# Performance work log

Measured on AMD Instinct MI355X. Metric: run time of the kernel, lower is better.

## Reference

```python
import jax, jax.numpy as jnp
import numpy as np

N = 4096      # nodes
IN = 45       # input_dim
H = 44        # hidden_dim
NH = 4        # num_heads
HD = H // NH  # head_dim = 11
E = 131072    # edges
SCALE = 0.1
NEG = -1e9


def _linear_params(key, fan_in, fan_out):
    kw, kb = jax.random.split(key)
    s = 1.0 / np.sqrt(fan_in)
    W = jax.random.uniform(kw, (fan_in, fan_out), jnp.float32, -s, s)
    b = jax.random.uniform(kb, (fan_out,), jnp.float32, -s, s)
    return W, b


def setup_inputs() -> dict:
    key = jax.random.key(0)
    ks = jax.random.split(key, 9)
    node_features = jax.random.normal(ks[0], (N, IN), jnp.float32)
    edge_index = jax.random.randint(ks[1], (2, E), 0, N, jnp.int32)
    # dt_minutes must be nonnegative (sqrt); channel 1 unused by forward
    temporal_data = jax.random.uniform(ks[2], (N, N, 2), jnp.float32, 0.01, 60.0)
    Wp, bp = _linear_params(ks[3], IN, H)
    Wq, bq = _linear_params(ks[4], H, H)
    Wk, bk = _linear_params(ks[5], H, H)
    Wv, bv = _linear_params(ks[6], H, H)
    Wo, bo = _linear_params(ks[7], H, H)
    return dict(node_features=node_features, edge_index=edge_index,
                temporal_data=temporal_data, Wp=Wp, bp=bp, Wq=Wq, bq=bq,
                Wk=Wk, bk=bk, Wv=Wv, bv=bv, Wo=Wo, bo=bo)


def reference(node_features, edge_index, temporal_data,
              Wp, bp, Wq, bq, Wk, bk, Wv, bv, Wo, bo):
    # input projection (N > 1000 so dag_positional_encoding is skipped)
    x = node_features @ Wp + bp                       # [N, H]
    # per-head QKV: [NH, N, HD]
    Q = (x @ Wq + bq).reshape(N, NH, HD).transpose(1, 0, 2)
    K = (x @ Wk + bk).reshape(N, NH, HD).transpose(1, 0, 2)
    V = (x @ Wv + bv).reshape(N, NH, HD).transpose(1, 0, 2)
    # edge mask: True blocks attention; edges and self-loops are allowed
    mask = jnp.ones((N, N), dtype=bool)
    mask = mask.at[edge_index[0], edge_index[1]].set(False)
    diag = jnp.arange(N)
    mask = mask.at[diag, diag].set(False)
    # rbf temporal bias: -sqrt(dt / (scale + 1e-6))
    tb = -jnp.sqrt(temporal_data[:, :, 0] / (SCALE + 1e-6))  # [N, N]
    scores = jnp.einsum('hnd,hmd->hnm', Q, K) / np.sqrt(HD)  # [NH, N, N]
    scores = scores + tb[None]
    scores = jnp.where(mask[None], NEG, scores)
    attn = jax.nn.softmax(scores, axis=-1)
    out = jnp.einsum('hnm,hmd->hnd', attn, V)                # [NH, N, HD]
    attended = out.transpose(1, 0, 2).reshape(N, H)          # [N, H]
    return attended @ Wo + bo
```

## Files before the change

kernel.cpp:

```cpp
#include <hip/hip_runtime.h>
#include <math.h>

#define NN 4096
#define INDIM 45
#define HH 44
#define NHEAD 4
#define HD 11
#define NEDGE 131072
#define CAP 128
#define MASKW (NN / 64)
#define NPB 8
#define RPITCH 66
#define KVSTRIDE 24

typedef unsigned short ushort_t;

__device__ __forceinline__ float wsum64(float v) {
    #pragma unroll
    for (int i = 32; i > 0; i >>= 1) v += __shfl_xor(v, i, 64);
    return v;
}
__device__ __forceinline__ float wmax64(float v) {
    #pragma unroll
    for (int i = 32; i > 0; i >>= 1) v = fmaxf(v, __shfl_xor(v, i, 64));
    return v;
}
__device__ __forceinline__ ushort_t f2bf(float x) {
    unsigned u = __float_as_uint(x);
    u += 0x7FFFu + ((u >> 16) & 1u);
    return (ushort_t)(u >> 16);
}
__device__ __forceinline__ float bfl(unsigned u) { return __uint_as_float(u << 16); }
__device__ __forceinline__ float bfh(unsigned u) { return __uint_as_float(u & 0xFFFF0000u); }

__global__ __launch_bounds__(256)
void proj_zero(const float* __restrict__ nf,
               const float* __restrict__ Wp, const float* __restrict__ bp,
               const float* __restrict__ Wq, const float* __restrict__ bq,
               const float* __restrict__ Wk, const float* __restrict__ bk,
               const float* __restrict__ Wv, const float* __restrict__ bv,
               unsigned long long* __restrict__ mask,
               float* __restrict__ Qp, ushort_t* __restrict__ KVb) {
    const int tid = threadIdx.x;
    const int gsz = gridDim.x * 256;
    for (int i = blockIdx.x * 256 + tid; i < NN * MASKW; i += gsz) mask[i] = 0ull;

    __shared__ float xs[NPB][HH];
    const int n0 = blockIdx.x * NPB;
    for (int idx = tid; idx < NPB * HH; idx += 256) {
        int nl = idx / HH, j = idx - nl * HH;
        const float* row = nf + (size_t)(n0 + nl) * INDIM;
        float a = bp[j];
        #pragma unroll
        for (int k = 0; k < INDIM; ++k) a += row[k] * Wp[k * HH + j];
        xs[nl][j] = a;
    }
    __syncthreads();
    for (int idx = tid; idx < NPB * HH; idx += 256) {
        int nl = idx / HH, j = idx - nl * HH;
        const float* row = xs[nl];
        float aq = bq[j], ak = bk[j], av = bv[j];
        #pragma unroll
        for (int k = 0; k < HH; ++k) {
            float xv = row[k];
            aq += xv * Wq[k * HH + j];
            ak += xv * Wk[k * HH + j];
            av += xv * Wv[k * HH + j];
        }
        int h = j / HD, d = j - h * HD;
        size_t nh = (size_t)(n0 + nl) * NHEAD + h;
        Qp[nh * 12 + d]             = aq;
        KVb[nh * KVSTRIDE + d]      = f2bf(ak);
        KVb[nh * KVSTRIDE + 12 + d] = f2bf(av);
    }
}

__global__ __launch_bounds__(256)
void build_mask(const int* __restrict__ ei, unsigned long long* __restrict__ mask) {
    int i = blockIdx.x * blockDim.x + threadIdx.x;
    if (i < NEDGE) {
        int r = ei[i];
        int c = ei[NEDGE + i];
        atomicOr(&mask[(size_t)r * MASKW + (c >> 6)], 1ull << (c & 63));
    }
}

__global__ __launch_bounds__(256, 6)
void attn_out(const float* __restrict__ Qp, const ushort_t* __restrict__ KVb,
              const float* __restrict__ temporal,
              const unsigned long long* __restrict__ mask,
              const float* __restrict__ Wo, const float* __restrict__ bo,
              float* __restrict__ out) {
    const int tid = threadIdx.x;
    const int lane = tid & 63;
    const int h = tid >> 6;
    const int n = blockIdx.x;
    const float scale = 0.30151134457776363f;
    const float tbmul = 9.99990000099999f;

    __shared__ int cols_s[NHEAD][CAP];
    __shared__ float red_s[NHEAD][12][RPITCH];
    __shared__ float att_s[HH];

    unsigned long long w = mask[(size_t)n * MASKW + lane];
    if (lane == (n >> 6)) w |= 1ull << (n & 63);
    int c = __popcll(w);
    int inc = c;
    #pragma unroll
    for (int i = 1; i < 64; i <<= 1) {
        int v = __shfl_up(inc, i, 64);
        if (lane >= i) inc += v;
    }
    int off = inc - c;
    int deg = __shfl(inc, 63, 64);
    if (deg > CAP) deg = CAP;
    while (w) {
        int b = __builtin_ctzll(w);
        w &= w - 1;
        if (off < CAP) cols_s[h][off] = lane * 64 + b;
        ++off;
    }

    const float4* qp4 = (const float4*)(Qp + ((size_t)n * NHEAD + h) * 12);
    float4 q0 = qp4[0], q1 = qp4[1], q2 = qp4[2];

    if (deg <= 64) {
        const bool act = lane < deg;
        const int col = act ? cols_s[h][lane] : cols_s[h][0];
        float t = temporal[((size_t)n * NN + col) * 2];
        const uint4* kv4 = (const uint4*)(KVb + (size_t)(col * NHEAD + h) * KVSTRIDE);
        uint4 A = kv4[0], B = kv4[1], C = kv4[2];
        float s = q0.x*bfl(A.x) + q0.y*bfh(A.x) + q0.z*bfl(A.y) + q0.w*bfh(A.y)
                + q1.x*bfl(A.z) + q1.y*bfh(A.z) + q1.z*bfl(A.w) + q1.w*bfh(A.w)
                + q2.x*bfl(B.x) + q2.y*bfh(B.x) + q2.z*bfl(B.y);
        float p = act ? __expf(s * scale - sqrtf(t * tbmul)) : 0.f;
        float vv[11] = { bfl(B.z), bfh(B.z), bfl(B.w), bfh(B.w),
                         bfl(C.x), bfh(C.x), bfl(C.y), bfh(C.y),
                         bfl(C.z), bfh(C.z), bfl(C.w) };

        float* myred = &red_s[h][0][0];
        #pragma unroll
        for (int d = 0; d < HD; ++d) myred[d * RPITCH + lane] = p * vv[d];
        myred[11 * RPITCH + lane] = p;
        int dd = lane < 12 ? lane : 0;
        const float2* rp = (const float2*)(myred + dd * RPITCH);
        float sum = 0.f;
        #pragma unroll
        for (int i = 0; i < 32; ++i) { float2 v2 = rp[i]; sum += v2.x + v2.y; }
        float inv = 1.f / __shfl(sum, 11, 64);
        if (lane < HD) att_s[h * HD + lane] = sum * inv;
    } else {
        float mcur = -INFINITY, lsum = 0.f, oacc[HD];
        #pragma unroll
        for (int d = 0; d < HD; ++d) oacc[d] = 0.f;
        for (int base = 0; base < deg; base += 64) {
            const int jj = base + lane;
            const bool act = jj < deg;
            const int col = act ? cols_s[h][jj] : 0;
            float t = temporal[((size_t)n * NN + col) * 2];
            const uint4* kv4 = (const uint4*)(KVb + (size_t)(col * NHEAD + h) * KVSTRIDE);
            uint4 A = kv4[0], B = kv4[1], C = kv4[2];
            float s = q0.x*bfl(A.x) + q0.y*bfh(A.x) + q0.z*bfl(A.y) + q0.w*bfh(A.y)
                    + q1.x*bfl(A.z) + q1.y*bfh(A.z) + q1.z*bfl(A.w) + q1.w*bfh(A.w)
                    + q2.x*bfl(B.x) + q2.y*bfh(B.x) + q2.z*bfl(B.y);
            float vv[11] = { bfl(B.z), bfh(B.z), bfl(B.w), bfh(B.w),
                             bfl(C.x), bfh(C.x), bfl(C.y), bfh(C.y),
                             bfl(C.z), bfh(C.z), bfl(C.w) };
            if (act) {
                s = s * scale - sqrtf(t * tbmul);
                if (s > mcur) {
                    float f = __expf(mcur - s);
                    lsum *= f;
                    #pragma unroll
                    for (int d = 0; d < HD; ++d) oacc[d] *= f;
                    mcur = s;
                }
                float p = __expf(s - mcur);
                lsum += p;
                #pragma unroll
                for (int d = 0; d < HD; ++d) oacc[d] += p * vv[d];
            }
        }
        float M = wmax64(mcur);
        float sc = (mcur == -INFINITY) ? 0.f : __expf(mcur - M);
        float L = wsum64(lsum * sc);
        float inv = 1.f / L;
        #pragma unroll
        for (int d = 0; d < HD; ++d) {
            float o = wsum64(oacc[d] * sc);
            if (lane == d) att_s[h * HD + d] = o * inv;
        }
    }
    __syncthreads();

    if (tid < HH) {
        float a = bo[tid];
        #pragma unroll
        for (int k = 0; k < HH; ++k) a += att_s[k] * Wo[k * HH + tid];
        out[(size_t)n * HH + tid] = a;
    }
}

extern "C" void kernel_launch(void* const* d_in, const int* in_sizes, int n_in,
                              void* d_out, int out_size, void* d_ws, size_t ws_size,
                              hipStream_t stream) {
    const float* nf       = (const float*)d_in[0];
    const int*   ei       = (const int*)d_in[1];
    const float* temporal = (const float*)d_in[2];
    const float* Wp = (const float*)d_in[3];
    const float* bp = (const float*)d_in[4];
    const float* Wq = (const float*)d_in[5];
    const float* bq = (const float*)d_in[6];
    const float* Wk = (const float*)d_in[7];
    const float* bk = (const float*)d_in[8];
    const float* Wv = (const float*)d_in[9];
    const float* bv = (const float*)d_in[10];
    const float* Wo = (const float*)d_in[11];
    const float* bo = (const float*)d_in[12];
    float* outp = (float*)d_out;

    char* ws = (char*)d_ws;
    unsigned long long* mask = (unsigned long long*)ws;
    float*    Qp  = (float*)(ws + (2u << 20));
    ushort_t* KVb = (ushort_t*)(Qp + (size_t)NN * NHEAD * 12);

    proj_zero<<<NN / NPB, 256, 0, stream>>>(nf, Wp, bp, Wq, bq, Wk, bk, Wv, bv,
                                            mask, Qp, KVb);
    build_mask<<<(NEDGE + 255) / 256, 256, 0, stream>>>(ei, mask);
    attn_out<<<NN, 256, 0, stream>>>(Qp, KVb, temporal, mask, Wo, bo, outp);
}
```

Measured before the change: 33.65 us.

## Split attention into per-head 64-thread blocks and separate output projection kernel

The attention kernel now launches one 64-thread block per (node, head) instead of one 256-thread block per node, which removes the block-wide barrier and lets heads schedule independently. Attended values go to a workspace buffer, and a new kernel applies the Wo projection. In exchange there is an extra kernel launch and a global round-trip for the attended tensor. The mask word popcount and scan are now repeated per head-block, though they already ran once per wavefront before.

```diff
diff --git a/kernel.cpp b/kernel.cpp
--- a/kernel.cpp
+++ b/kernel.cpp
@@ -85,22 +85,22 @@
     }
 }
 
-__global__ __launch_bounds__(256, 6)
-void attn_out(const float* __restrict__ Qp, const ushort_t* __restrict__ KVb,
-              const float* __restrict__ temporal,
-              const unsigned long long* __restrict__ mask,
-              const float* __restrict__ Wo, const float* __restrict__ bo,
-              float* __restrict__ out) {
-    const int tid = threadIdx.x;
-    const int lane = tid & 63;
-    const int h = tid >> 6;
-    const int n = blockIdx.x;
+__global__ __launch_bounds__(64, 6)
+void attn64(const float* __restrict__ Qp, const ushort_t* __restrict__ KVb,
+            const float* __restrict__ temporal,
+            const unsigned long long* __restrict__ mask,
+            float* __restrict__ att) {
+    const int lane = threadIdx.x;
+    const int n = blockIdx.x >> 2;
+    const int h = blockIdx.x & 3;
     const float scale = 0.30151134457776363f;
     const float tbmul = 9.99990000099999f;
 
-    __shared__ int cols_s[NHEAD][CAP];
-    __shared__ float red_s[NHEAD][12][RPITCH];
-    __shared__ float att_s[HH];
+    __shared__ int cols_s[CAP];
+    __shared__ float red_s[12][RPITCH];
+
+    const float4* qp4 = (const float4*)(Qp + ((size_t)n * NHEAD + h) * 12);
+    float4 q0 = qp4[0], q1 = qp4[1], q2 = qp4[2];
 
     unsigned long long w = mask[(size_t)n * MASKW + lane];
     if (lane == (n >> 6)) w |= 1ull << (n & 63);
@@ -117,16 +117,13 @@
     while (w) {
         int b = __builtin_ctzll(w);
         w &= w - 1;
-        if (off < CAP) cols_s[h][off] = lane * 64 + b;
+        if (off < CAP) cols_s[off] = lane * 64 + b;
         ++off;
     }
-
-    const float4* qp4 = (const float4*)(Qp + ((size_t)n * NHEAD + h) * 12);
-    float4 q0 = qp4[0], q1 = qp4[1], q2 = qp4[2];
 
     if (deg <= 64) {
         const bool act = lane < deg;
-        const int col = act ? cols_s[h][lane] : cols_s[h][0];
+        const int col = act ? cols_s[lane] : cols_s[0];
         float t = temporal[((size_t)n * NN + col) * 2];
         const uint4* kv4 = (const uint4*)(KVb + (size_t)(col * NHEAD + h) * KVSTRIDE);
         uint4 A = kv4[0], B = kv4[1], C = kv4[2];
@@ -138,17 +135,16 @@
                          bfl(C.x), bfh(C.x), bfl(C.y), bfh(C.y),
                          bfl(C.z), bfh(C.z), bfl(C.w) };
 
-        float* myred = &red_s[h][0][0];
-        #pragma unroll
-        for (int d = 0; d < HD; ++d) myred[d * RPITCH + lane] = p * vv[d];
-        myred[11 * RPITCH + lane] = p;
+        #pragma unroll
+        for (int d = 0; d < HD; ++d) red_s[d][lane] = p * vv[d];
+        red_s[11][lane] = p;
         int dd = lane < 12 ? lane : 0;
-        const float2* rp = (const float2*)(myred + dd * RPITCH);
+        const float2* rp = (const float2*)(&red_s[dd][0]);
         float sum = 0.f;
         #pragma unroll
         for (int i = 0; i < 32; ++i) { float2 v2 = rp[i]; sum += v2.x + v2.y; }
         float inv = 1.f / __shfl(sum, 11, 64);
-        if (lane < HD) att_s[h * HD + lane] = sum * inv;
+        if (lane < HD) att[(size_t)n * HH + h * HD + lane] = sum * inv;
     } else {
         float mcur = -INFINITY, lsum = 0.f, oacc[HD];
         #pragma unroll
@@ -156,7 +152,7 @@
         for (int base = 0; base < deg; base += 64) {
             const int jj = base + lane;
             const bool act = jj < deg;
-            const int col = act ? cols_s[h][jj] : 0;
+            const int col = act ? cols_s[jj] : 0;
             float t = temporal[((size_t)n * NN + col) * 2];
             const uint4* kv4 = (const uint4*)(KVb + (size_t)(col * NHEAD + h) * KVSTRIDE);
             uint4 A = kv4[0], B = kv4[1], C = kv4[2];
@@ -188,17 +184,22 @@
         #pragma unroll
         for (int d = 0; d < HD; ++d) {
             float o = wsum64(oacc[d] * sc);
-            if (lane == d) att_s[h * HD + d] = o * inv;
+            if (lane == d) att[(size_t)n * HH + h * HD + d] = o * inv;
         }
     }
-    __syncthreads();
-
-    if (tid < HH) {
-        float a = bo[tid];
-        #pragma unroll
-        for (int k = 0; k < HH; ++k) a += att_s[k] * Wo[k * HH + tid];
-        out[(size_t)n * HH + tid] = a;
-    }
+}
+
+__global__ __launch_bounds__(256)
+void proj_out(const float* __restrict__ att, const float* __restrict__ Wo,
+              const float* __restrict__ bo, float* __restrict__ out) {
+    int idx = blockIdx.x * 256 + threadIdx.x;
+    if (idx >= NN * HH) return;
+    int n = idx / HH, j = idx - n * HH;
+    const float* row = att + (size_t)n * HH;
+    float a = bo[j];
+    #pragma unroll
+    for (int k = 0; k < HH; ++k) a += row[k] * Wo[k * HH + j];
+    out[idx] = a;
 }
 
 extern "C" void kernel_launch(void* const* d_in, const int* in_sizes, int n_in,
@@ -223,9 +224,11 @@
     unsigned long long* mask = (unsigned long long*)ws;
     float*    Qp  = (float*)(ws + (2u << 20));
     ushort_t* KVb = (ushort_t*)(Qp + (size_t)NN * NHEAD * 12);
+    float*    att = (float*)(KVb + (size_t)NN * NHEAD * KVSTRIDE);
 
     proj_zero<<<NN / NPB, 256, 0, stream>>>(nf, Wp, bp, Wq, bq, Wk, bk, Wv, bv,
                                             mask, Qp, KVb);
     build_mask<<<(NEDGE + 255) / 256, 256, 0, stream>>>(ei, mask);
-    attn_out<<<NN, 256, 0, stream>>>(Qp, KVb, temporal, mask, Wo, bo, outp);
-}
+    attn64<<<NN * NHEAD, 64, 0, stream>>>(Qp, KVb, temporal, mask, att);
+    proj_out<<<(NN * HH + 255) / 256, 256, 0, stream>>>(att, Wo, bo, outp);
+}
```

Measured after the change: 40.72 us. 1.21x slower.
